# Optimization experiments

Measured on AMD Instinct MI355X. Metric: run time of the kernel, lower is better.

## Reference

```python
import jax, jax.numpy as jnp
import numpy as np

B, S, K, D, H, COND, MR = 4, 1024, 1024, 1024, 16, 1024, 4
HD = D // H  # 64
INV_SQRT_HD = 1.0 / float(np.sqrt(HD))
GELU_C = 0.7978845608028654  # sqrt(2/pi)


def _make_rope(seqlen):
    pos = jnp.arange(seqlen, dtype=jnp.float32)
    inv = 1.0 / (10000.0 ** (jnp.arange(0, HD // 2, dtype=jnp.float32) * 2.0 / HD))
    ang = pos[:, None] * inv[None, :]                     # [S, HD/2]
    cos = jnp.concatenate([jnp.cos(ang), jnp.cos(ang)], -1)  # [S, HD]
    sin = jnp.concatenate([jnp.sin(ang), jnp.sin(ang)], -1)
    return cos[None, :, None, :], sin[None, :, None, :]   # [1,S,1,HD]


def setup_inputs():
    key = jax.random.key(0)
    ks = jax.random.split(key, 14)
    rn = lambda k, shape, s=0.02: jax.random.normal(k, shape, jnp.float32) * s
    cos_q, sin_q = _make_rope(S)
    cos_k, sin_k = _make_rope(K)
    ada_b = jnp.zeros((6 * D,), jnp.float32)
    ada_b = ada_b.at[2 * D:3 * D].set(0.5).at[5 * D:6 * D].set(0.5)  # gate_msa, gate_mlp init
    return {
        "q_x": jax.random.normal(ks[0], (B, S, D), jnp.float32),
        "kv_x": jax.random.normal(ks[1], (B, K, D), jnp.float32),
        "t_cond": jax.random.normal(ks[2], (B, COND), jnp.float32),
        "cos_q": cos_q, "sin_q": sin_q, "cos_k": cos_k, "sin_k": sin_k,
        "group_idxs": jax.random.randint(ks[3], (B, S), 0, 4, jnp.int32),
        "query_enabled": jax.random.randint(ks[4], (B, S), 0, 2, jnp.int32).astype(bool),
        "qn_w": jnp.ones((D,), jnp.float32),
        "kvn_w": jnp.ones((D,), jnp.float32),
        "n2_w": jnp.ones((D,), jnp.float32),
        "Wq": rn(ks[5], (D, D)), "Wkv": rn(ks[6], (D, 2 * D)), "Wo": rn(ks[7], (D, D)),
        "W1": rn(ks[8], (D, MR * D)), "b1": jnp.zeros((MR * D,), jnp.float32),
        "W2": rn(ks[9], (MR * D, D)), "b2": jnp.zeros((D,), jnp.float32),
        "adaW": rn(ks[10], (COND, 6 * D)), "adab": ada_b,
    }


def layer_norm(x, w):
    mu = jnp.mean(x, -1, keepdims=True)
    var = jnp.var(x, -1, keepdims=True)
    return (x - mu) * jax.lax.rsqrt(var + 1e-5) * w


def rope(x, cos, sin):
    # x: [B,S,H,HD]; cos/sin: [1,S,1,HD]; rotate_half convention
    x1, x2 = jnp.split(x, 2, axis=-1)
    return x * cos + jnp.concatenate([-x2, x1], -1) * sin


def gelu_tanh(x):
    return 0.5 * x * (1.0 + jnp.tanh(GELU_C * (x + 0.044715 * x * x * x)))


def reference(q_x, kv_x, t_cond, cos_q, sin_q, cos_k, sin_k, group_idxs, query_enabled,
              qn_w, kvn_w, n2_w, Wq, Wkv, Wo, W1, b1, W2, b2, adaW, adab):
    # adaLN modulation (inference: dropout disabled -> bias_dropout_add_scale = scale*x + residual)
    mod = (t_cond @ adaW + adab)[:, None, :]               # [B,1,6D]
    sh_msa, sc_msa, g_msa, sh_mlp, sc_mlp, g_mlp = jnp.split(mod, 6, axis=-1)

    qn = layer_norm(q_x, qn_w)
    kvn = layer_norm(kv_x, kvn_w)
    qn = qn * (1.0 + sc_msa) + sh_msa                      # modulate_fused

    q = (qn @ Wq).reshape(B, S, H, HD)
    kv = (kvn @ Wkv).reshape(B, K, 2, H, HD)
    k, v = kv[:, :, 0], kv[:, :, 1]
    q = rope(q, cos_q, sin_q)
    k = rope(k, cos_k, sin_k)

    # group cross-attn mask: attend only where groups differ
    attend = group_idxs[:, :, None] != group_idxs[:, None, :]  # [B,S,K]
    scores = jnp.einsum('bqhd,bkhd->bhqk', q, k) * INV_SQRT_HD
    scores = jnp.where(attend[:, None, :, :], scores, -1e9)
    p = jax.nn.softmax(scores, axis=-1)
    attn = jnp.einsum('bhqk,bkhd->bqhd', p, v).reshape(B, S, D)

    x = g_msa * (attn @ Wo) + q_x                          # fused bias-dropout-add-scale (inference)
    gate = query_enabled[..., None].astype(x.dtype)
    x = x * gate + q_x * (1.0 - gate)                      # gated_update

    x_mid = x
    h = layer_norm(x, n2_w) * (1.0 + sc_mlp) + sh_mlp
    h = gelu_tanh(h @ W1 + b1) @ W2 + b2
    x = g_mlp * h + x_mid
    x = x * gate + x_mid * (1.0 - gate)
    return x
```

## Files before the change

### kernel.cpp

```cpp
#include <hip/hip_runtime.h>
#include <hip/hip_bf16.h>
#include <math.h>

typedef __bf16 bf16_t;
typedef __attribute__((ext_vector_type(8))) __bf16 bf16x8;
typedef __attribute__((ext_vector_type(4))) __bf16 bf16x4;
typedef __attribute__((ext_vector_type(4))) float f32x4;

__global__ __launch_bounds__(256) void compact_kernel(
    const int* __restrict__ qen, int* __restrict__ idx, int* __restrict__ McPtr)
{
  __shared__ int cnts[256];
  int t = threadIdx.x;
  int flags[16], c = 0;
#pragma unroll
  for (int i = 0; i < 16; ++i) {
    flags[i] = qen[t * 16 + i] != 0;
    c += flags[i];
  }
  cnts[t] = c;
  __syncthreads();
  for (int off = 1; off < 256; off <<= 1) {
    int v = cnts[t];
    if (t >= off) v += cnts[t - off];
    __syncthreads();
    cnts[t] = v;
    __syncthreads();
  }
  int p = cnts[t] - c;
  int total = cnts[255];
#pragma unroll
  for (int i = 0; i < 16; ++i)
    if (flags[i]) idx[p++] = t * 16 + i;
  if (t == 0) *McPtr = total;
  for (int j = total + t; j < 4096; j += 256) idx[j] = 0;
}

__global__ __launch_bounds__(256) void copy_disabled_kernel(
    const int* __restrict__ qen, const float* __restrict__ qx,
    float* __restrict__ out)
{
  int row = blockIdx.x;
  if (qen[row]) return;
  int tid = threadIdx.x;
  ((float4*)(out + (size_t)row * 1024))[tid] =
      ((const float4*)(qx + (size_t)row * 1024))[tid];
}

__global__ __launch_bounds__(256) void mod_init_kernel(
    const float* __restrict__ adab, float* __restrict__ mod)
{
  int i = blockIdx.x * 256 + threadIdx.x;
  mod[i] = adab[i % 6144];
}

__global__ __launch_bounds__(256) void mod_partial_kernel(
    const float* __restrict__ tc, const float* __restrict__ adaW,
    float* __restrict__ mod)
{
  __shared__ float st[4][128];
  int tid = threadIdx.x, z = blockIdx.y;
  for (int i = tid; i < 512; i += 256)
    st[i >> 7][i & 127] = tc[(i >> 7) * 1024 + z * 128 + (i & 127)];
  __syncthreads();
  int col = blockIdx.x * 256 + tid;
  float a0 = 0.f, a1 = 0.f, a2 = 0.f, a3 = 0.f;
  for (int k = 0; k < 128; ++k) {
    float wv = adaW[(size_t)(z * 128 + k) * 6144 + col];
    a0 = fmaf(st[0][k], wv, a0);
    a1 = fmaf(st[1][k], wv, a1);
    a2 = fmaf(st[2][k], wv, a2);
    a3 = fmaf(st[3][k], wv, a3);
  }
  atomicAdd(&mod[col], a0);
  atomicAdd(&mod[6144 + col], a1);
  atomicAdd(&mod[2 * 6144 + col], a2);
  atomicAdd(&mod[3 * 6144 + col], a3);
}

__global__ __launch_bounds__(256) void transpose_all(
    const float* __restrict__ Wq, const float* __restrict__ Wkv,
    const float* __restrict__ Wo, const float* __restrict__ W1,
    const float* __restrict__ W2,
    bf16_t* __restrict__ oWq, bf16_t* __restrict__ oWkv,
    bf16_t* __restrict__ oWo, bf16_t* __restrict__ oW1,
    bf16_t* __restrict__ oW2)
{
  __shared__ float tile[32][33];
  int bid = blockIdx.x;
  const float* in; bf16_t* out; int R, C, gx, local;
  if (bid < 1024)      { in = Wq;  out = oWq;  R = 1024; C = 1024; gx = 32;  local = bid; }
  else if (bid < 3072) { in = Wkv; out = oWkv; R = 1024; C = 2048; gx = 64;  local = bid - 1024; }
  else if (bid < 4096) { in = Wo;  out = oWo;  R = 1024; C = 1024; gx = 32;  local = bid - 3072; }
  else if (bid < 8192) { in = W1;  out = oW1;  R = 1024; C = 4096; gx = 128; local = bid - 4096; }
  else                 { in = W2;  out = oW2;  R = 4096; C = 1024; gx = 32;  local = bid - 8192; }
  int c0 = (local % gx) * 32, r0 = (local / gx) * 32;
  int tx = threadIdx.x, ty = threadIdx.y;
#pragma unroll
  for (int i = 0; i < 4; ++i)
    tile[ty + i * 8][tx] = in[(size_t)(r0 + ty + i * 8) * C + c0 + tx];
  __syncthreads();
#pragma unroll
  for (int i = 0; i < 4; ++i)
    out[(size_t)(c0 + ty + i * 8) * R + r0 + tx] = (bf16_t)tile[tx][ty + i * 8];
}

__global__ __launch_bounds__(256) void ln_both_kernel(
    const float* __restrict__ qx, const float* __restrict__ kvx,
    const float* __restrict__ qnw, const float* __restrict__ kvnw,
    const float* __restrict__ mod,
    bf16_t* __restrict__ qn_out, bf16_t* __restrict__ kvn_out)
{
  int rowg = blockIdx.x;
  bool isQ = rowg < 4096;
  int row = isQ ? rowg : rowg - 4096;
  int b = row >> 10;
  int tid = threadIdx.x;
  const float* x = (isQ ? qx : kvx) + (size_t)row * 1024;
  const float* wgt = isQ ? qnw : kvnw;
  bf16_t* outp = (isQ ? qn_out : kvn_out) + (size_t)row * 1024;

  float4 v = ((const float4*)x)[tid];
  float s = v.x + v.y + v.z + v.w;
  float s2 = v.x * v.x + v.y * v.y + v.z * v.z + v.w * v.w;
#pragma unroll
  for (int off = 32; off > 0; off >>= 1) {
    s += __shfl_down(s, off, 64);
    s2 += __shfl_down(s2, off, 64);
  }
  __shared__ float ps[4], ps2[4];
  if ((tid & 63) == 0) { ps[tid >> 6] = s; ps2[tid >> 6] = s2; }
  __syncthreads();
  float mu = (ps[0] + ps[1] + ps[2] + ps[3]) * (1.0f / 1024.0f);
  float var = (ps2[0] + ps2[1] + ps2[2] + ps2[3]) * (1.0f / 1024.0f) - mu * mu;
  float rs = rsqrtf(var + 1e-5f);
  float xv[4] = {v.x, v.y, v.z, v.w};
#pragma unroll
  for (int i = 0; i < 4; ++i) {
    int col = tid * 4 + i;
    float n = (xv[i] - mu) * rs * wgt[col];
    if (isQ)
      n = n * (1.0f + mod[b * 6144 + 1024 + col]) + mod[b * 6144 + col];
    outp[col] = (bf16_t)n;
  }
}

__global__ __launch_bounds__(256) void reduce_q_rope_kernel(
    const bf16_t* __restrict__ P0, const bf16_t* __restrict__ P1,
    const float* __restrict__ cosq, const float* __restrict__ sinq,
    bf16_t* __restrict__ qr)
{
  int t = blockIdx.x * 256 + threadIdx.x;
  int hd = t & 31;
  int h = (t >> 5) & 15;
  int s = (t >> 9) & 1023;
  int b = t >> 19;
  size_t base = ((size_t)(b * 1024 + s)) * 1024 + h * 64 + hd;
  float v1 = (float)P0[base] + (float)P1[base];
  float v2 = (float)P0[base + 32] + (float)P1[base + 32];
  float c1 = cosq[s * 64 + hd], s1 = sinq[s * 64 + hd];
  float c2 = cosq[s * 64 + hd + 32], s2 = sinq[s * 64 + hd + 32];
  float o1 = (v1 * c1 - v2 * s1) * 0.125f;
  float o2 = (v2 * c2 + v1 * s2) * 0.125f;
  size_t ob = ((size_t)(b * 16 + h) * 1024 + s) * 64 + hd;
  qr[ob] = (bf16_t)o1;
  qr[ob + 32] = (bf16_t)o2;
}

__global__ __launch_bounds__(256) void reduce_kv_kernel(
    const bf16_t* __restrict__ P0, const bf16_t* __restrict__ P1,
    const float* __restrict__ cosk, const float* __restrict__ sink,
    bf16_t* __restrict__ kr, bf16_t* __restrict__ vt)
{
  __shared__ float ks[64][65];
  __shared__ float vs[64][65];
  int bh = blockIdx.x;
  int b = bh >> 4, h = bh & 15;
  int n0 = blockIdx.y * 64;
  int tid = threadIdx.x;
#pragma unroll
  for (int it = 0; it < 16; ++it) {
    int linear = tid + it * 256;
    int nl = linear >> 6, hd = linear & 63;
    size_t gi = ((size_t)(b * 1024 + n0 + nl)) * 2048 + h * 64 + hd;
    ks[nl][hd] = (float)P0[gi] + (float)P1[gi];
    vs[hd][nl] = (float)P0[gi + 1024] + (float)P1[gi + 1024];
  }
  __syncthreads();
#pragma unroll
  for (int it = 0; it < 16; ++it) {
    int linear = tid + it * 256;
    int nl = linear >> 6, hd = linear & 63;
    float kv = ks[nl][hd];
    float pv = ks[nl][hd ^ 32];
    float c = cosk[(n0 + nl) * 64 + hd], sn = sink[(n0 + nl) * 64 + hd];
    float o = (hd < 32) ? (kv * c - pv * sn) : (kv * c + pv * sn);
    kr[((size_t)bh * 1024 + n0 + nl) * 64 + hd] = (bf16_t)o;
    vt[((size_t)bh * 64 + nl) * 1024 + n0 + hd] = (bf16_t)vs[nl][hd];
  }
}

__global__ __launch_bounds__(256, 4) void attn_kernel(
    const bf16_t* __restrict__ qr, const bf16_t* __restrict__ kr,
    const bf16_t* __restrict__ vt, const int* __restrict__ grp,
    bf16_t* __restrict__ outp)
{
  __shared__ bf16_t Ks[64 * 68];
  __shared__ bf16_t Vs[64 * 68];
  __shared__ bf16_t Ps[64 * 68];
  __shared__ int gk[64];
  const int bh = blockIdx.x;
  const int b = bh >> 4, h = bh & 15;
  const int qBase = blockIdx.y * 64;
  const int tid = threadIdx.x, lane = tid & 63, w = tid >> 6;
  const int l15 = lane & 15, l4 = lane >> 4;
  const f32x4 zero = {0.f, 0.f, 0.f, 0.f};

  const int qrow = qBase + w * 16;
  const bf16_t* qp = qr + ((size_t)bh * 1024 + qrow + l15) * 64;
  bf16x8 qA0 = *(const bf16x8*)(qp + l4 * 8);
  bf16x8 qA1 = *(const bf16x8*)(qp + 32 + l4 * 8);
  int gqr[4];
#pragma unroll
  for (int r = 0; r < 4; ++r) gqr[r] = grp[b * 1024 + qrow + l4 * 4 + r];

  f32x4 oacc[4];
  float rsum[4];
#pragma unroll
  for (int i = 0; i < 4; ++i) { oacc[i] = zero; rsum[i] = 0.f; }

  for (int kt = 0; kt < 16; ++kt) {
    __syncthreads();
#pragma unroll
    for (int i = 0; i < 2; ++i) {
      int c = tid * 2 + i;
      int r = c >> 3, cc = (c & 7) * 8;
      *(bf16x8*)(Ks + r * 68 + cc) =
          *(const bf16x8*)(kr + ((size_t)bh * 1024 + kt * 64 + r) * 64 + cc);
      *(bf16x8*)(Vs + r * 68 + cc) =
          *(const bf16x8*)(vt + ((size_t)bh * 64 + r) * 1024 + kt * 64 + cc);
    }
    if (tid < 64) gk[tid] = grp[b * 1024 + kt * 64 + tid];
    __syncthreads();

    f32x4 sacc[4];
#pragma unroll
    for (int nt = 0; nt < 4; ++nt) sacc[nt] = zero;
#pragma unroll
    for (int nt = 0; nt < 4; ++nt) {
      bf16x8 kf0 = *(const bf16x8*)(Ks + (nt * 16 + l15) * 68 + l4 * 8);
      bf16x8 kf1 = *(const bf16x8*)(Ks + (nt * 16 + l15) * 68 + 32 + l4 * 8);
      sacc[nt] = __builtin_amdgcn_mfma_f32_16x16x32_bf16(qA0, kf0, sacc[nt], 0, 0, 0);
      sacc[nt] = __builtin_amdgcn_mfma_f32_16x16x32_bf16(qA1, kf1, sacc[nt], 0, 0, 0);
    }
#pragma unroll
    for (int r = 0; r < 4; ++r) {
      int gq = gqr[r];
      float acc = 0.f;
#pragma unroll
      for (int nt = 0; nt < 4; ++nt) {
        float sv = sacc[nt][r] + ((gq == gk[nt * 16 + l15]) ? -60.f : 0.f);
        float p = __expf(sv);
        acc += p;
        Ps[(w * 16 + l4 * 4 + r) * 68 + nt * 16 + l15] = (bf16_t)p;
      }
      rsum[r] += acc;
    }
    const bf16_t* pp = Ps + (w * 16 + l15) * 68;
    bf16x8 pf0 = *(const bf16x8*)(pp + l4 * 8);
    bf16x8 pf1 = *(const bf16x8*)(pp + 32 + l4 * 8);
#pragma unroll
    for (int nt = 0; nt < 4; ++nt) {
      bf16x8 vf0 = *(const bf16x8*)(Vs + (nt * 16 + l15) * 68 + l4 * 8);
      bf16x8 vf1 = *(const bf16x8*)(Vs + (nt * 16 + l15) * 68 + 32 + l4 * 8);
      oacc[nt] = __builtin_amdgcn_mfma_f32_16x16x32_bf16(pf0, vf0, oacc[nt], 0, 0, 0);
      oacc[nt] = __builtin_amdgcn_mfma_f32_16x16x32_bf16(pf1, vf1, oacc[nt], 0, 0, 0);
    }
  }

#pragma unroll
  for (int r = 0; r < 4; ++r) {
    float t = rsum[r];
    t += __shfl_xor(t, 1, 64);
    t += __shfl_xor(t, 2, 64);
    t += __shfl_xor(t, 4, 64);
    t += __shfl_xor(t, 8, 64);
    float inv = 1.f / t;
    int srow = qBase + w * 16 + l4 * 4 + r;
#pragma unroll
    for (int nt = 0; nt < 4; ++nt)
      outp[((size_t)(b * 1024 + srow)) * 1024 + h * 64 + nt * 16 + l15] =
          (bf16_t)(oacc[nt][r] * inv);
  }
}

__device__ __forceinline__ void stage16(const bf16_t* gp, bf16_t* lp) {
  __builtin_amdgcn_global_load_lds(
      (__attribute__((address_space(1))) void*)gp,
      (__attribute__((address_space(3))) void*)lp, 16, 0, 0);
}

__global__ __launch_bounds__(256, 2) void gemm_qkv(
    const bf16_t* __restrict__ qn, const bf16_t* __restrict__ WqT,
    const bf16_t* __restrict__ kvn, const bf16_t* __restrict__ WkvT,
    bf16_t* __restrict__ scr)
{
  __shared__ bf16_t sA[128 * 64];
  __shared__ bf16_t sB[128 * 64];
  const int tid = threadIdx.x;
  const int lane = tid & 63, w = tid >> 6;
  const int wr = w >> 1, wc = w & 1;
  const int z = blockIdx.z;

  const int L = blockIdx.y * 24 + blockIdx.x;
  const int xcd = L & 7, id2 = L >> 3;
  const int tileY = (xcd & 3) * 8 + (id2 % 8);
  const int tileX = (xcd >> 2) * 12 + (id2 / 8);
  const int rowBase = tileY * 128;

  const bf16_t* A;
  const bf16_t* Bt;
  bf16_t* Cb;
  int N, colBase;
  size_t zOff;
  if (tileX < 8) {
    A = qn; Bt = WqT; N = 1024; colBase = tileX * 128;
    Cb = scr; zOff = (size_t)z * 4194304;
  } else {
    A = kvn; Bt = WkvT; N = 2048; colBase = (tileX - 8) * 128;
    Cb = scr + 8388608; zOff = (size_t)z * 8388608;
  }

  const int l15 = lane & 15, l4 = lane >> 4;
  const int srow = lane >> 3;
  const int sg = lane & 7;
  const int scol = (sg ^ srow) * 8;
  const int rl = l15 & 7;
  const int g0 = (l4 ^ rl) * 8;
  const int g1 = ((4 + l4) ^ rl) * 8;

  const f32x4 zero = {0.f, 0.f, 0.f, 0.f};
  f32x4 acc[4][4];
#pragma unroll
  for (int i = 0; i < 4; ++i)
#pragma unroll
    for (int j = 0; j < 4; ++j) acc[i][j] = zero;

  const bf16_t* aBase = A + (size_t)(rowBase + w * 32 + srow) * 1024 + scol;
  const bf16_t* bBase = Bt + (size_t)(colBase + w * 32 + srow) * 1024 + scol;

  const int kStart = z * 512;
  for (int k0 = kStart; k0 < kStart + 512; k0 += 64) {
    __syncthreads();
#pragma unroll
    for (int i = 0; i < 4; ++i) {
      stage16(aBase + (size_t)i * 8 * 1024 + k0, sA + (w * 32 + i * 8) * 64);
      stage16(bBase + (size_t)i * 8 * 1024 + k0, sB + (w * 32 + i * 8) * 64);
    }
    __syncthreads();
    bf16x8 af[4], bfr[4];
#pragma unroll
    for (int mt = 0; mt < 4; ++mt)
      af[mt] = *(const bf16x8*)(sA + (wr * 64 + mt * 16 + l15) * 64 + g0);
#pragma unroll
    for (int nt = 0; nt < 4; ++nt)
      bfr[nt] = *(const bf16x8*)(sB + (wc * 64 + nt * 16 + l15) * 64 + g0);
#pragma unroll
    for (int mt = 0; mt < 4; ++mt)
#pragma unroll
      for (int nt = 0; nt < 4; ++nt)
        acc[mt][nt] = __builtin_amdgcn_mfma_f32_16x16x32_bf16(af[mt], bfr[nt],
                                                              acc[mt][nt], 0, 0, 0);
#pragma unroll
    for (int mt = 0; mt < 4; ++mt)
      af[mt] = *(const bf16x8*)(sA + (wr * 64 + mt * 16 + l15) * 64 + g1);
#pragma unroll
    for (int nt = 0; nt < 4; ++nt)
      bfr[nt] = *(const bf16x8*)(sB + (wc * 64 + nt * 16 + l15) * 64 + g1);
#pragma unroll
    for (int mt = 0; mt < 4; ++mt)
#pragma unroll
      for (int nt = 0; nt < 4; ++nt)
        acc[mt][nt] = __builtin_amdgcn_mfma_f32_16x16x32_bf16(af[mt], bfr[nt],
                                                              acc[mt][nt], 0, 0, 0);
  }

#pragma unroll
  for (int mt = 0; mt < 4; ++mt)
#pragma unroll
    for (int nt = 0; nt < 4; ++nt) {
      int col = colBase + wc * 64 + nt * 16 + l15;
#pragma unroll
      for (int r = 0; r < 4; ++r) {
        int rr = rowBase + wr * 64 + mt * 16 + l4 * 4 + r;
        Cb[zOff + (size_t)rr * N + col] = (bf16_t)acc[mt][nt][r];
      }
    }
}

template <int EPI, int GATHER>
__global__ __launch_bounds__(256, 2) void gemm64_c(
    const bf16_t* __restrict__ A, const bf16_t* __restrict__ Bt,
    int N, int Kd, int kChunk, bf16_t* __restrict__ Cb,
    const float* __restrict__ bias,
    const int* __restrict__ idxG, const int* __restrict__ McPtr)
{
  __shared__ bf16_t sA[64 * 64];
  __shared__ bf16_t sB[128 * 64];
  const int Mc = *McPtr;
  const int gx = gridDim.x;
  const int L = blockIdx.y * gx + blockIdx.x;
  const int xcd = L & 7, id2 = L >> 3;
  const int tileY = (id2 / gx) * 8 + xcd;
  const int tileX = id2 % gx;
  const int rowBase = tileY * 64;
  if (rowBase >= Mc) return;
  const int colBase = tileX * 128;

  const int tid = threadIdx.x;
  const int lane = tid & 63, w = tid >> 6;
  const int wr = w >> 1, wc = w & 1;
  const int l15 = lane & 15, l4 = lane >> 4;
  const int srow = lane >> 3;
  const int sg = lane & 7;
  const int scol = (sg ^ srow) * 8;
  const int rl = l15 & 7;
  const int g0 = (l4 ^ rl) * 8;
  const int g1 = ((4 + l4) ^ rl) * 8;

  const f32x4 zero = {0.f, 0.f, 0.f, 0.f};
  f32x4 acc[2][4];
#pragma unroll
  for (int i = 0; i < 2; ++i)
#pragma unroll
    for (int j = 0; j < 4; ++j) acc[i][j] = zero;

  const bf16_t* aB[2];
#pragma unroll
  for (int i = 0; i < 2; ++i) {
    int rowc = rowBase + w * 16 + i * 8 + srow;
    int arow = GATHER ? idxG[rowc] : rowc;
    aB[i] = A + (size_t)arow * Kd + scol;
  }
  const bf16_t* bBase = Bt + (size_t)(colBase + w * 32 + srow) * Kd + scol;

  const int kStart = blockIdx.z * kChunk;
  for (int k0 = kStart; k0 < kStart + kChunk; k0 += 64) {
    __syncthreads();
#pragma unroll
    for (int i = 0; i < 2; ++i)
      stage16(aB[i] + k0, sA + (w * 16 + i * 8) * 64);
#pragma unroll
    for (int i = 0; i < 4; ++i)
      stage16(bBase + (size_t)i * 8 * Kd + k0, sB + (w * 32 + i * 8) * 64);
    __syncthreads();
    bf16x8 af[2], bfr[4];
#pragma unroll
    for (int mt = 0; mt < 2; ++mt)
      af[mt] = *(const bf16x8*)(sA + (wr * 32 + mt * 16 + l15) * 64 + g0);
#pragma unroll
    for (int nt = 0; nt < 4; ++nt)
      bfr[nt] = *(const bf16x8*)(sB + (wc * 64 + nt * 16 + l15) * 64 + g0);
#pragma unroll
    for (int mt = 0; mt < 2; ++mt)
#pragma unroll
      for (int nt = 0; nt < 4; ++nt)
        acc[mt][nt] = __builtin_amdgcn_mfma_f32_16x16x32_bf16(af[mt], bfr[nt],
                                                              acc[mt][nt], 0, 0, 0);
#pragma unroll
    for (int mt = 0; mt < 2; ++mt)
      af[mt] = *(const bf16x8*)(sA + (wr * 32 + mt * 16 + l15) * 64 + g1);
#pragma unroll
    for (int nt = 0; nt < 4; ++nt)
      bfr[nt] = *(const bf16x8*)(sB + (wc * 64 + nt * 16 + l15) * 64 + g1);
#pragma unroll
    for (int mt = 0; mt < 2; ++mt)
#pragma unroll
      for (int nt = 0; nt < 4; ++nt)
        acc[mt][nt] = __builtin_amdgcn_mfma_f32_16x16x32_bf16(af[mt], bfr[nt],
                                                              acc[mt][nt], 0, 0, 0);
  }

  const size_t zOff = (size_t)blockIdx.z * 4096 * N;
#pragma unroll
  for (int mt = 0; mt < 2; ++mt)
#pragma unroll
    for (int nt = 0; nt < 4; ++nt) {
      int col = colBase + wc * 64 + nt * 16 + l15;
#pragma unroll
      for (int r = 0; r < 4; ++r) {
        int rr = rowBase + wr * 32 + mt * 16 + l4 * 4 + r;
        float v = acc[mt][nt][r];
        if constexpr (EPI == 1) {
          float t = v + bias[col];
          float zz = 0.7978845608028654f * (t + 0.044715f * t * t * t);
          float e = __expf(2.f * zz);
          float g = 0.5f * t * (2.f - 2.f / (e + 1.f));
          Cb[(size_t)rr * N + col] = (bf16_t)g;
        } else {
          Cb[zOff + (size_t)rr * N + col] = (bf16_t)v;
        }
      }
    }
}

__global__ __launch_bounds__(256) void ln2_fused_kernel(
    const bf16_t* __restrict__ P, const float* __restrict__ qx,
    const float* __restrict__ n2w, const float* __restrict__ mod,
    const int* __restrict__ idxG, const int* __restrict__ McPtr,
    float* __restrict__ xbufc, bf16_t* __restrict__ xnc)
{
  int rowc = blockIdx.x;
  if (rowc >= *McPtr) return;
  int rr = idxG[rowc];
  int b = rr >> 10;
  int tid = threadIdx.x;
  size_t rc = (size_t)rowc * 1024 + tid * 4;
  bf16x4 p0 = *(const bf16x4*)(P + rc);
  bf16x4 p1 = *(const bf16x4*)(P + 4194304 + rc);
  bf16x4 p2 = *(const bf16x4*)(P + 2 * 4194304 + rc);
  bf16x4 p3 = *(const bf16x4*)(P + 3 * 4194304 + rc);
  float4 res = ((const float4*)(qx + (size_t)rr * 1024))[tid];
  float4 g = ((const float4*)(mod + b * 6144 + 2048))[tid];
  float4 x;
  x.x = fmaf(g.x, (float)p0[0] + (float)p1[0] + (float)p2[0] + (float)p3[0], res.x);
  x.y = fmaf(g.y, (float)p0[1] + (float)p1[1] + (float)p2[1] + (float)p3[1], res.y);
  x.z = fmaf(g.z, (float)p0[2] + (float)p1[2] + (float)p2[2] + (float)p3[2], res.z);
  x.w = fmaf(g.w, (float)p0[3] + (float)p1[3] + (float)p2[3] + (float)p3[3], res.w);
  *(float4*)(xbufc + rc) = x;

  float s = x.x + x.y + x.z + x.w;
  float s2 = x.x * x.x + x.y * x.y + x.z * x.z + x.w * x.w;
#pragma unroll
  for (int off = 32; off > 0; off >>= 1) {
    s += __shfl_down(s, off, 64);
    s2 += __shfl_down(s2, off, 64);
  }
  __shared__ float ps[4], ps2[4];
  if ((tid & 63) == 0) { ps[tid >> 6] = s; ps2[tid >> 6] = s2; }
  __syncthreads();
  float mu = (ps[0] + ps[1] + ps[2] + ps[3]) * (1.0f / 1024.0f);
  float var = (ps2[0] + ps2[1] + ps2[2] + ps2[3]) * (1.0f / 1024.0f) - mu * mu;
  float rs = rsqrtf(var + 1e-5f);
  float4 sc = ((const float4*)(mod + b * 6144 + 4096))[tid];
  float4 sh = ((const float4*)(mod + b * 6144 + 3072))[tid];
  float4 wv = ((const float4*)n2w)[tid];
  float xv[4] = {x.x, x.y, x.z, x.w};
  float scv[4] = {sc.x, sc.y, sc.z, sc.w};
  float shv[4] = {sh.x, sh.y, sh.z, sh.w};
  float wvv[4] = {wv.x, wv.y, wv.z, wv.w};
#pragma unroll
  for (int i = 0; i < 4; ++i) {
    float n = (xv[i] - mu) * rs * wvv[i];
    n = n * (1.0f + scv[i]) + shv[i];
    xnc[(size_t)rowc * 1024 + tid * 4 + i] = (bf16_t)n;
  }
}

__global__ __launch_bounds__(256) void final_reduce_kernel(
    const bf16_t* __restrict__ P, const float* __restrict__ b2,
    const float* __restrict__ mod, const int* __restrict__ idxG,
    const int* __restrict__ McPtr, const float* __restrict__ xbufc,
    float* __restrict__ out)
{
  int rowc = blockIdx.x;
  if (rowc >= *McPtr) return;
  int rr = idxG[rowc];
  int b = rr >> 10;
  int tid = threadIdx.x;
  size_t rc = (size_t)rowc * 1024 + tid * 4;
  bf16x4 p0 = *(const bf16x4*)(P + rc);
  bf16x4 p1 = *(const bf16x4*)(P + 4194304 + rc);
  bf16x4 p2 = *(const bf16x4*)(P + 2 * 4194304 + rc);
  bf16x4 p3 = *(const bf16x4*)(P + 3 * 4194304 + rc);
  float4 bb = ((const float4*)b2)[tid];
  float4 xm = *(const float4*)(xbufc + rc);
  float4 g = ((const float4*)(mod + b * 6144 + 5120))[tid];
  float v0 = (float)p0[0] + (float)p1[0] + (float)p2[0] + (float)p3[0] + bb.x;
  float v1 = (float)p0[1] + (float)p1[1] + (float)p2[1] + (float)p3[1] + bb.y;
  float v2 = (float)p0[2] + (float)p1[2] + (float)p2[2] + (float)p3[2] + bb.z;
  float v3 = (float)p0[3] + (float)p1[3] + (float)p2[3] + (float)p3[3] + bb.w;
  float4 o;
  o.x = fmaf(g.x, v0, xm.x);
  o.y = fmaf(g.y, v1, xm.y);
  o.z = fmaf(g.z, v2, xm.z);
  o.w = fmaf(g.w, v3, xm.w);
  *(float4*)(out + (size_t)rr * 1024 + tid * 4) = o;
}

extern "C" void kernel_launch(void* const* d_in, const int* in_sizes, int n_in,
                              void* d_out, int out_size, void* d_ws, size_t ws_size,
                              hipStream_t stream)
{
  const float* q_x    = (const float*)d_in[0];
  const float* kv_x   = (const float*)d_in[1];
  const float* t_cond = (const float*)d_in[2];
  const float* cos_q  = (const float*)d_in[3];
  const float* sin_q  = (const float*)d_in[4];
  const float* cos_k  = (const float*)d_in[5];
  const float* sin_k  = (const float*)d_in[6];
  const int*   grp    = (const int*)d_in[7];
  const int*   qen    = (const int*)d_in[8];
  const float* qn_w   = (const float*)d_in[9];
  const float* kvn_w  = (const float*)d_in[10];
  const float* n2_w   = (const float*)d_in[11];
  const float* Wq     = (const float*)d_in[12];
  const float* Wkv    = (const float*)d_in[13];
  const float* Wo     = (const float*)d_in[14];
  const float* W1     = (const float*)d_in[15];
  const float* b1     = (const float*)d_in[16];
  const float* W2     = (const float*)d_in[17];
  const float* b2     = (const float*)d_in[18];
  const float* adaW   = (const float*)d_in[19];
  const float* adab   = (const float*)d_in[20];
  float* out = (float*)d_out;

  char* ws = (char*)d_ws;
  const size_t MB = 1ull << 20;
  float*  mod    = (float*)(ws + 0);
  int*    idxL   = (int*)(ws + 98304);
  int*    McPtr  = (int*)(ws + 98304 + 16384);
  char*   wbase  = ws + 131072;
  bf16_t* Wq_t   = (bf16_t*)(wbase);
  bf16_t* Wkv_t  = (bf16_t*)(wbase + 2 * MB);
  bf16_t* Wo_t   = (bf16_t*)(wbase + 6 * MB);
  bf16_t* W1_t   = (bf16_t*)(wbase + 8 * MB);
  bf16_t* W2_t   = (bf16_t*)(wbase + 16 * MB);
  bf16_t* qn_mod = (bf16_t*)(wbase + 24 * MB);
  bf16_t* kvn    = (bf16_t*)(wbase + 32 * MB);
  bf16_t* q_r    = (bf16_t*)(wbase + 40 * MB);
  bf16_t* k_r    = (bf16_t*)(wbase + 48 * MB);
  bf16_t* v_t    = (bf16_t*)(wbase + 56 * MB);
  bf16_t* h1     = (bf16_t*)(wbase + 64 * MB);
  bf16_t* scr    = (bf16_t*)(wbase + 96 * MB);
  bf16_t* xn_c   = qn_mod;
  bf16_t* attn_o = kvn;
  float*  xbuf_c = (float*)q_r;

  compact_kernel<<<1, 256, 0, stream>>>(qen, idxL, McPtr);
  copy_disabled_kernel<<<4096, 256, 0, stream>>>(qen, q_x, out);
  mod_init_kernel<<<96, 256, 0, stream>>>(adab, mod);
  mod_partial_kernel<<<dim3(24, 8), 256, 0, stream>>>(t_cond, adaW, mod);
  transpose_all<<<12288, dim3(32, 8), 0, stream>>>(Wq, Wkv, Wo, W1, W2,
                                                   Wq_t, Wkv_t, Wo_t, W1_t, W2_t);
  ln_both_kernel<<<8192, 256, 0, stream>>>(q_x, kv_x, qn_w, kvn_w, mod,
                                           qn_mod, kvn);
  gemm_qkv<<<dim3(24, 32, 2), 256, 0, stream>>>(qn_mod, Wq_t, kvn, Wkv_t, scr);
  reduce_q_rope_kernel<<<8192, 256, 0, stream>>>(scr, scr + 4194304, cos_q, sin_q, q_r);
  reduce_kv_kernel<<<dim3(64, 16), 256, 0, stream>>>(scr + 8388608, scr + 16777216,
                                                     cos_k, sin_k, k_r, v_t);
  attn_kernel<<<dim3(64, 16), 256, 0, stream>>>(q_r, k_r, v_t, grp, attn_o);
  gemm64_c<4, 1><<<dim3(8, 64, 4), 256, 0, stream>>>(attn_o, Wo_t, 1024, 1024, 256,
                                                     scr, nullptr, idxL, McPtr);
  ln2_fused_kernel<<<4096, 256, 0, stream>>>(scr, q_x, n2_w, mod, idxL, McPtr,
                                             xbuf_c, xn_c);
  gemm64_c<1, 0><<<dim3(32, 64, 1), 256, 0, stream>>>(xn_c, W1_t, 4096, 1024, 1024,
                                                      h1, b1, idxL, McPtr);
  gemm64_c<4, 0><<<dim3(8, 64, 4), 256, 0, stream>>>(h1, W2_t, 1024, 4096, 1024,
                                                     scr, nullptr, idxL, McPtr);
  final_reduce_kernel<<<4096, 256, 0, stream>>>(scr, b2, mod, idxL, McPtr, xbuf_c, out);
}
```

Before: 411.8 us.

## Rewrite attention to keep P in registers via transposed QK and fp16 PV MFMA

The attention kernel now computes S^T = K·Q^T so the MFMA output layout directly feeds the fp16 16x16x16 MFMA as the P operand. This removes the LDS round-trip for P and the K/V LDS staging with its block barriers; K, V and group ids are loaded straight from global memory into registers. Each wave now handles 32 query rows (two 16-row sub-tiles), halving the grid, and V is stored as fp16 instead of bf16. The trade-off is higher register pressure (launch bounds lowered to 2), redundant global loads of K/V per wave without LDS sharing, and fp16 range risk for V/P values.

```diff
diff --git a/kernel.cpp b/kernel.cpp
--- a/kernel.cpp
+++ b/kernel.cpp
@@ -3,8 +3,10 @@
 #include <math.h>
 
 typedef __bf16 bf16_t;
+typedef __fp16 f16_t;
 typedef __attribute__((ext_vector_type(8))) __bf16 bf16x8;
 typedef __attribute__((ext_vector_type(4))) __bf16 bf16x4;
+typedef __attribute__((ext_vector_type(4))) __fp16 f16x4;
 typedef __attribute__((ext_vector_type(4))) float f32x4;
 
 __global__ __launch_bounds__(256) void compact_kernel(
@@ -170,7 +172,7 @@
 __global__ __launch_bounds__(256) void reduce_kv_kernel(
     const bf16_t* __restrict__ P0, const bf16_t* __restrict__ P1,
     const float* __restrict__ cosk, const float* __restrict__ sink,
-    bf16_t* __restrict__ kr, bf16_t* __restrict__ vt)
+    bf16_t* __restrict__ kr, f16_t* __restrict__ vt)
 {
   __shared__ float ks[64][65];
   __shared__ float vs[64][65];
@@ -196,101 +198,106 @@
     float c = cosk[(n0 + nl) * 64 + hd], sn = sink[(n0 + nl) * 64 + hd];
     float o = (hd < 32) ? (kv * c - pv * sn) : (kv * c + pv * sn);
     kr[((size_t)bh * 1024 + n0 + nl) * 64 + hd] = (bf16_t)o;
-    vt[((size_t)bh * 64 + nl) * 1024 + n0 + hd] = (bf16_t)vs[nl][hd];
-  }
-}
-
-__global__ __launch_bounds__(256, 4) void attn_kernel(
+    vt[((size_t)bh * 64 + nl) * 1024 + n0 + hd] = (f16_t)vs[nl][hd];
+  }
+}
+
+__global__ __launch_bounds__(256, 2) void attn_kernel(
     const bf16_t* __restrict__ qr, const bf16_t* __restrict__ kr,
-    const bf16_t* __restrict__ vt, const int* __restrict__ grp,
+    const f16_t* __restrict__ vt, const int* __restrict__ grp,
     bf16_t* __restrict__ outp)
 {
-  __shared__ bf16_t Ks[64 * 68];
-  __shared__ bf16_t Vs[64 * 68];
-  __shared__ bf16_t Ps[64 * 68];
-  __shared__ int gk[64];
   const int bh = blockIdx.x;
   const int b = bh >> 4, h = bh & 15;
-  const int qBase = blockIdx.y * 64;
+  const int qBase = blockIdx.y * 128;
   const int tid = threadIdx.x, lane = tid & 63, w = tid >> 6;
   const int l15 = lane & 15, l4 = lane >> 4;
   const f32x4 zero = {0.f, 0.f, 0.f, 0.f};
 
-  const int qrow = qBase + w * 16;
-  const bf16_t* qp = qr + ((size_t)bh * 1024 + qrow + l15) * 64;
-  bf16x8 qA0 = *(const bf16x8*)(qp + l4 * 8);
-  bf16x8 qA1 = *(const bf16x8*)(qp + 32 + l4 * 8);
-  int gqr[4];
-#pragma unroll
-  for (int r = 0; r < 4; ++r) gqr[r] = grp[b * 1024 + qrow + l4 * 4 + r];
-
-  f32x4 oacc[4];
-  float rsum[4];
-#pragma unroll
-  for (int i = 0; i < 4; ++i) { oacc[i] = zero; rsum[i] = 0.f; }
+  bf16x8 qB0[2], qB1[2];
+  int gq[2];
+#pragma unroll
+  for (int s = 0; s < 2; ++s) {
+    int qrow = qBase + w * 32 + s * 16;
+    const bf16_t* qp = qr + ((size_t)bh * 1024 + qrow + l15) * 64;
+    qB0[s] = *(const bf16x8*)(qp + l4 * 8);
+    qB1[s] = *(const bf16x8*)(qp + 32 + l4 * 8);
+    gq[s] = grp[b * 1024 + qrow + l15];
+  }
+
+  f32x4 oacc[2][4];
+  float rsum[2] = {0.f, 0.f};
+#pragma unroll
+  for (int s = 0; s < 2; ++s)
+#pragma unroll
+    for (int d = 0; d < 4; ++d) oacc[s][d] = zero;
 
   for (int kt = 0; kt < 16; ++kt) {
-    __syncthreads();
-#pragma unroll
-    for (int i = 0; i < 2; ++i) {
-      int c = tid * 2 + i;
-      int r = c >> 3, cc = (c & 7) * 8;
-      *(bf16x8*)(Ks + r * 68 + cc) =
-          *(const bf16x8*)(kr + ((size_t)bh * 1024 + kt * 64 + r) * 64 + cc);
-      *(bf16x8*)(Vs + r * 68 + cc) =
-          *(const bf16x8*)(vt + ((size_t)bh * 64 + r) * 1024 + kt * 64 + cc);
+    bf16x8 kA0[4], kA1[4];
+    int4 gkv[4];
+#pragma unroll
+    for (int nt = 0; nt < 4; ++nt) {
+      const bf16_t* kp = kr + ((size_t)bh * 1024 + kt * 64 + nt * 16 + l15) * 64;
+      kA0[nt] = *(const bf16x8*)(kp + l4 * 8);
+      kA1[nt] = *(const bf16x8*)(kp + 32 + l4 * 8);
+      gkv[nt] = *(const int4*)(grp + b * 1024 + kt * 64 + nt * 16 + l4 * 4);
     }
-    if (tid < 64) gk[tid] = grp[b * 1024 + kt * 64 + tid];
-    __syncthreads();
-
-    f32x4 sacc[4];
-#pragma unroll
-    for (int nt = 0; nt < 4; ++nt) sacc[nt] = zero;
-#pragma unroll
-    for (int nt = 0; nt < 4; ++nt) {
-      bf16x8 kf0 = *(const bf16x8*)(Ks + (nt * 16 + l15) * 68 + l4 * 8);
-      bf16x8 kf1 = *(const bf16x8*)(Ks + (nt * 16 + l15) * 68 + 32 + l4 * 8);
-      sacc[nt] = __builtin_amdgcn_mfma_f32_16x16x32_bf16(qA0, kf0, sacc[nt], 0, 0, 0);
-      sacc[nt] = __builtin_amdgcn_mfma_f32_16x16x32_bf16(qA1, kf1, sacc[nt], 0, 0, 0);
+    f16x4 vf[4][4];
+#pragma unroll
+    for (int ntd = 0; ntd < 4; ++ntd)
+#pragma unroll
+      for (int ntk = 0; ntk < 4; ++ntk)
+        vf[ntd][ntk] = *(const f16x4*)(
+            vt + ((size_t)bh * 64 + ntd * 16 + l15) * 1024 + kt * 64 +
+            ntk * 16 + l4 * 4);
+
+#pragma unroll
+    for (int s = 0; s < 2; ++s) {
+      f16x4 pT[4];
+      float acc = 0.f;
+#pragma unroll
+      for (int ntk = 0; ntk < 4; ++ntk) {
+        f32x4 sacc = zero;
+        sacc = __builtin_amdgcn_mfma_f32_16x16x32_bf16(kA0[ntk], qB0[s], sacc, 0, 0, 0);
+        sacc = __builtin_amdgcn_mfma_f32_16x16x32_bf16(kA1[ntk], qB1[s], sacc, 0, 0, 0);
+        f16x4 p;
+        int gqs = gq[s];
+#pragma unroll
+        for (int r = 0; r < 4; ++r) {
+          int gk = (r == 0) ? gkv[ntk].x : (r == 1) ? gkv[ntk].y
+                   : (r == 2) ? gkv[ntk].z : gkv[ntk].w;
+          float sv = sacc[r] + ((gqs == gk) ? -60.f : 0.f);
+          float pe = __expf(sv);
+          acc += pe;
+          p[r] = (f16_t)pe;
+        }
+        pT[ntk] = p;
+      }
+      rsum[s] += acc;
+#pragma unroll
+      for (int ntd = 0; ntd < 4; ++ntd)
+#pragma unroll
+        for (int ntk = 0; ntk < 4; ++ntk)
+          oacc[s][ntd] = __builtin_amdgcn_mfma_f32_16x16x16f16(
+              pT[ntk], vf[ntd][ntk], oacc[s][ntd], 0, 0, 0);
     }
+  }
+
+#pragma unroll
+  for (int s = 0; s < 2; ++s) {
+    float t = rsum[s];
+    t += __shfl_xor(t, 16, 64);
+    t += __shfl_xor(t, 32, 64);
+    float tinv = 1.f / t;
 #pragma unroll
     for (int r = 0; r < 4; ++r) {
-      int gq = gqr[r];
-      float acc = 0.f;
-#pragma unroll
-      for (int nt = 0; nt < 4; ++nt) {
-        float sv = sacc[nt][r] + ((gq == gk[nt * 16 + l15]) ? -60.f : 0.f);
-        float p = __expf(sv);
-        acc += p;
-        Ps[(w * 16 + l4 * 4 + r) * 68 + nt * 16 + l15] = (bf16_t)p;
-      }
-      rsum[r] += acc;
+      float inv = __shfl(tinv, l4 * 4 + r, 64);
+      int srow = qBase + w * 32 + s * 16 + l4 * 4 + r;
+#pragma unroll
+      for (int ntd = 0; ntd < 4; ++ntd)
+        outp[((size_t)(b * 1024 + srow)) * 1024 + h * 64 + ntd * 16 + l15] =
+            (bf16_t)(oacc[s][ntd][r] * inv);
     }
-    const bf16_t* pp = Ps + (w * 16 + l15) * 68;
-    bf16x8 pf0 = *(const bf16x8*)(pp + l4 * 8);
-    bf16x8 pf1 = *(const bf16x8*)(pp + 32 + l4 * 8);
-#pragma unroll
-    for (int nt = 0; nt < 4; ++nt) {
-      bf16x8 vf0 = *(const bf16x8*)(Vs + (nt * 16 + l15) * 68 + l4 * 8);
-      bf16x8 vf1 = *(const bf16x8*)(Vs + (nt * 16 + l15) * 68 + 32 + l4 * 8);
-      oacc[nt] = __builtin_amdgcn_mfma_f32_16x16x32_bf16(pf0, vf0, oacc[nt], 0, 0, 0);
-      oacc[nt] = __builtin_amdgcn_mfma_f32_16x16x32_bf16(pf1, vf1, oacc[nt], 0, 0, 0);
-    }
-  }
-
-#pragma unroll
-  for (int r = 0; r < 4; ++r) {
-    float t = rsum[r];
-    t += __shfl_xor(t, 1, 64);
-    t += __shfl_xor(t, 2, 64);
-    t += __shfl_xor(t, 4, 64);
-    t += __shfl_xor(t, 8, 64);
-    float inv = 1.f / t;
-    int srow = qBase + w * 16 + l4 * 4 + r;
-#pragma unroll
-    for (int nt = 0; nt < 4; ++nt)
-      outp[((size_t)(b * 1024 + srow)) * 1024 + h * 64 + nt * 16 + l15] =
-          (bf16_t)(oacc[nt][r] * inv);
   }
 }
 
@@ -630,7 +637,7 @@
   bf16_t* kvn    = (bf16_t*)(wbase + 32 * MB);
   bf16_t* q_r    = (bf16_t*)(wbase + 40 * MB);
   bf16_t* k_r    = (bf16_t*)(wbase + 48 * MB);
-  bf16_t* v_t    = (bf16_t*)(wbase + 56 * MB);
+  f16_t*  v_t    = (f16_t*)(wbase + 56 * MB);
   bf16_t* h1     = (bf16_t*)(wbase + 64 * MB);
   bf16_t* scr    = (bf16_t*)(wbase + 96 * MB);
   bf16_t* xn_c   = qn_mod;
@@ -649,7 +656,7 @@
   reduce_q_rope_kernel<<<8192, 256, 0, stream>>>(scr, scr + 4194304, cos_q, sin_q, q_r);
   reduce_kv_kernel<<<dim3(64, 16), 256, 0, stream>>>(scr + 8388608, scr + 16777216,
                                                      cos_k, sin_k, k_r, v_t);
-  attn_kernel<<<dim3(64, 16), 256, 0, stream>>>(q_r, k_r, v_t, grp, attn_o);
+  attn_kernel<<<dim3(64, 8), 256, 0, stream>>>(q_r, k_r, v_t, grp, attn_o);
   gemm64_c<4, 1><<<dim3(8, 64, 4), 256, 0, stream>>>(attn_o, Wo_t, 1024, 1024, 256,
                                                      scr, nullptr, idxL, McPtr);
   ln2_fused_kernel<<<4096, 256, 0, stream>>>(scr, q_x, n2_w, mod, idxL, McPtr,
```

After: 434.1 us. +5.4%, slower.
